# Kernel tuning notes

Hardware: AMD Instinct MI355X
Metric: run time of the kernel (lower is better)

The kernel has to match this reference:

```python
import jax, jax.numpy as jnp
import numpy as np

N = 100000
NEG_SLOPE = 0.2

def _leaky_relu(x, slope):
    return jnp.where(x >= 0, x, slope * x)

def _gat_layer(h_in, W, a_src, a_dst, b, src, dst, heads, out_ch):
    # h: [N, H, C]
    h = (h_in @ W).reshape(-1, heads, out_ch)
    alpha_src = (h * a_src).sum(-1)  # [N, H]
    alpha_dst = (h * a_dst).sum(-1)  # [N, H]
    e = _leaky_relu(alpha_src[src] + alpha_dst[dst], NEG_SLOPE)  # [E, H]
    # segment softmax over destination nodes
    m = jax.ops.segment_max(e, dst, num_segments=N)
    m = jnp.where(jnp.isfinite(m), m, 0.0)
    ex = jnp.exp(e - m[dst])
    denom = jax.ops.segment_sum(ex, dst, num_segments=N)
    attn = ex / (denom[dst] + 1e-16)  # [E, H]
    out = jax.ops.segment_sum(h[src] * attn[:, :, None], dst, num_segments=N)  # [N, H, C]
    return out.reshape(-1, heads * out_ch) + b

def setup_inputs() -> dict:
    key = jax.random.key(0)
    ks = jax.random.split(key, 10)
    F_in, H1, C1, n_cls = 512, 8, 8, 16
    E = 1600000
    x = jax.random.normal(ks[0], (N, F_in), dtype=jnp.float32)
    edge_index = jax.random.randint(ks[1], (2, E), 0, N, dtype=jnp.int64)
    s1 = 1.0 / np.sqrt(F_in)
    W1 = jax.random.uniform(ks[2], (F_in, H1 * C1), jnp.float32, -s1, s1)
    a1_src = jax.random.normal(ks[3], (H1, C1), dtype=jnp.float32) * 0.1
    a1_dst = jax.random.normal(ks[4], (H1, C1), dtype=jnp.float32) * 0.1
    b1 = jnp.zeros((H1 * C1,), jnp.float32)
    s2 = 1.0 / np.sqrt(H1 * C1)
    W2 = jax.random.uniform(ks[5], (H1 * C1, n_cls), jnp.float32, -s2, s2)
    a2_src = jax.random.normal(ks[6], (1, n_cls), dtype=jnp.float32) * 0.1
    a2_dst = jax.random.normal(ks[7], (1, n_cls), dtype=jnp.float32) * 0.1
    b2 = jnp.zeros((n_cls,), jnp.float32)
    return {"x": x, "edge_index": edge_index, "W1": W1, "a1_src": a1_src,
            "a1_dst": a1_dst, "b1": b1, "W2": W2, "a2_src": a2_src,
            "a2_dst": a2_dst, "b2": b2}

def reference(x, edge_index, W1, a1_src, a1_dst, b1, W2, a2_src, a2_dst, b2):
    # add self loops (GATConv default)
    loops = jnp.arange(N, dtype=edge_index.dtype)
    src = jnp.concatenate([edge_index[0], loops])
    dst = jnp.concatenate([edge_index[1], loops])
    h = _gat_layer(x, W1, a1_src, a1_dst, b1, src, dst, 8, 8)
    h = jax.nn.elu(h)
    out = _gat_layer(h, W2, a2_src, a2_dst, b2, src, dst, 1, 16)
    return jax.nn.log_softmax(out, axis=1)
```

## Files before the change

kernel.cpp:

```cpp
#include <hip/hip_runtime.h>
#include <math.h>

#define NEG_SLOPE 0.2f
#define BKT_SHIFT 8
#define BKT_RANGE 256
#define EPB 4096

typedef __attribute__((ext_vector_type(8))) short bf16x8;
typedef __attribute__((ext_vector_type(4))) float f32x4;

__device__ __forceinline__ float elu1(float x)  { return x > 0.f ? x : expm1f(x); }

__device__ __forceinline__ unsigned short f2bf(float f) {
  unsigned u = __float_as_uint(f);
  unsigned r = (u + 0x7FFFu + ((u >> 16) & 1u)) >> 16;
  return (unsigned short)r;
}
__device__ __forceinline__ float bf2f(unsigned short s) {
  return __uint_as_float((unsigned)s << 16);
}
__device__ __forceinline__ float bflo(unsigned u) { return __uint_as_float(u << 16); }
__device__ __forceinline__ float bfhi(unsigned u) { return __uint_as_float(u & 0xFFFF0000u); }
__device__ __forceinline__ unsigned cvt_pk_bf16(float lo, float hi) {
  unsigned r;
  asm("v_cvt_pk_bf16_f32 %0, %1, %2" : "=v"(r) : "v"(lo), "v"(hi));
  return r;
}

__global__ __launch_bounds__(256) void k_cvtW(const float* __restrict__ W,
                                              unsigned short* __restrict__ Wt) {
  int i = blockIdx.x * 256 + threadIdx.x;
  if (i >= 512 * 64) return;
  int k = i >> 6, c = i & 63;
  Wt[(size_t)c * 512 + k] = f2bf(W[i]);
}

__global__ __launch_bounds__(256) void k_gemm1_mfma(const float* __restrict__ x,
                                                    const unsigned short* __restrict__ Wt,
                                                    unsigned short* __restrict__ h1b, int N) {
  __shared__ unsigned short As[128 * 64];
  __shared__ unsigned short Bs[64 * 64];
  const int t = threadIdx.x;
  const int w = t >> 6;
  const int l = t & 63;
  const int fr = l & 15;
  const int fq = l >> 4;
  const int rowbase = blockIdx.x * 128;
  f32x4 acc[2][4] = {};

  for (int k0 = 0; k0 < 512; k0 += 64) {
#pragma unroll
    for (int j = 0; j < 8; ++j) {
      int idx = j * 256 + t;
      int row = idx >> 4;
      int cg  = idx & 15;
      int grow = rowbase + row;
      float4 v = make_float4(0.f, 0.f, 0.f, 0.f);
      if (grow < N) v = *(const float4*)(x + (size_t)grow * 512 + k0 + cg * 4);
      uint2 pk;
      pk.x = cvt_pk_bf16(v.x, v.y);
      pk.y = cvt_pk_bf16(v.z, v.w);
      int ch = cg >> 1;
      int pch = ch ^ (row & 7);
      *((uint2*)(As + row * 64 + pch * 8 + (cg & 1) * 4)) = pk;
    }
#pragma unroll
    for (int rep = 0; rep < 2; ++rep) {
      int i = t + rep * 256;
      int c = i >> 3, ch = i & 7;
      uint4 v = *(const uint4*)(Wt + (size_t)c * 512 + k0 + ch * 8);
      *((uint4*)(Bs + c * 64 + (ch ^ (c & 7)) * 8)) = v;
    }
    __syncthreads();
#pragma unroll
    for (int ks = 0; ks < 2; ++ks) {
      bf16x8 a[2], b[4];
#pragma unroll
      for (int m = 0; m < 2; ++m) {
        int r = w * 32 + m * 16 + fr;
        int ch = (ks * 4 + fq) ^ (r & 7);
        a[m] = *((const bf16x8*)(As + r * 64 + ch * 8));
      }
#pragma unroll
      for (int n = 0; n < 4; ++n) {
        int c = n * 16 + fr;
        int ch = (ks * 4 + fq) ^ (c & 7);
        b[n] = *((const bf16x8*)(Bs + c * 64 + ch * 8));
      }
#pragma unroll
      for (int m = 0; m < 2; ++m)
#pragma unroll
        for (int n = 0; n < 4; ++n)
          acc[m][n] = __builtin_amdgcn_mfma_f32_16x16x32_bf16(a[m], b[n], acc[m][n], 0, 0, 0);
    }
    __syncthreads();
  }
#pragma unroll
  for (int m = 0; m < 2; ++m) {
    int rb = rowbase + w * 32 + m * 16 + fq * 4;
#pragma unroll
    for (int reg = 0; reg < 4; ++reg) {
      int row = rb + reg;
      if (row < N) {
#pragma unroll
        for (int n = 0; n < 4; ++n)
          h1b[(size_t)row * 64 + n * 16 + fr] = f2bf(acc[m][n][reg]);
      }
    }
  }
}

__global__ __launch_bounds__(256) void k_alpha1(const unsigned short* __restrict__ h1b,
                                                const float* __restrict__ a1s,
                                                const float* __restrict__ a1d,
                                                float* __restrict__ ef1s,
                                                float* __restrict__ ef1d, int N) {
  int idx = blockIdx.x * blockDim.x + threadIdx.x;
  if (idx >= N * 8) return;
  int h = idx & 7;
  uint4 raw = *(const uint4*)(h1b + (size_t)idx * 8);
  float v[8];
  v[0] = bflo(raw.x); v[1] = bfhi(raw.x);
  v[2] = bflo(raw.y); v[3] = bfhi(raw.y);
  v[4] = bflo(raw.z); v[5] = bfhi(raw.z);
  v[6] = bflo(raw.w); v[7] = bfhi(raw.w);
  const float* s_ = a1s + h * 8;
  const float* d_ = a1d + h * 8;
  float ss = 0.f, dd = 0.f;
#pragma unroll
  for (int j = 0; j < 8; ++j) { ss += v[j] * s_[j]; dd += v[j] * d_[j]; }
  *(float2*)(ef1s + (size_t)idx * 2) = make_float2(expf(ss), expf(NEG_SLOPE * ss));
  *(float2*)(ef1d + (size_t)idx * 2) = make_float2(expf(dd), expf(NEG_SLOPE * dd));
}

__global__ __launch_bounds__(512) void k_zero(int* __restrict__ p, int n) {
  int i = blockIdx.x * blockDim.x + threadIdx.x;
  if (i < n) p[i] = 0;
}

__global__ __launch_bounds__(256) void k_bhist(const int* __restrict__ dst,
                                               int* __restrict__ bucketCount,
                                               int E, int B) {
  __shared__ int h[512];
  int t = threadIdx.x;
  for (int i = t; i < B; i += 256) h[i] = 0;
  __syncthreads();
  int e0 = blockIdx.x * EPB;
#pragma unroll
  for (int i = 0; i < EPB / 256; ++i) {
    int e = e0 + i * 256 + t;
    if (e < E) atomicAdd(&h[dst[e] >> BKT_SHIFT], 1);
  }
  __syncthreads();
  for (int i = t; i < B; i += 256)
    if (h[i]) atomicAdd(bucketCount + i, h[i]);
}

__global__ __launch_bounds__(512) void k_bscan(const int* __restrict__ bucketCount,
                                               int* __restrict__ bucketOff,
                                               int* __restrict__ gCursor, int B, int E) {
  __shared__ int sm[512];
  int t = threadIdx.x;
  int v = (t < B) ? bucketCount[t] : 0;
  sm[t] = v;
  __syncthreads();
  int acc = v;
#pragma unroll
  for (int o = 1; o < 512; o <<= 1) {
    int u = (t >= o) ? sm[t - o] : 0;
    __syncthreads();
    acc += u;
    sm[t] = acc;
    __syncthreads();
  }
  if (t < B) {
    bucketOff[t] = acc - v;
    gCursor[t] = acc - v;
  }
  if (t == 0) bucketOff[B] = E;
}

__global__ __launch_bounds__(256) void k_bin(const int* __restrict__ src,
                                             const int* __restrict__ dst,
                                             int* __restrict__ gCursor,
                                             unsigned* __restrict__ binned,
                                             int E, int B) {
  __shared__ int hist[512];
  __shared__ int base[512];
  int t = threadIdx.x;
  for (int i = t; i < B; i += 256) hist[i] = 0;
  __syncthreads();
  int e0 = blockIdx.x * EPB;
#pragma unroll
  for (int i = 0; i < EPB / 256; ++i) {
    int e = e0 + i * 256 + t;
    if (e < E) atomicAdd(&hist[dst[e] >> BKT_SHIFT], 1);
  }
  __syncthreads();
  for (int i = t; i < B; i += 256) {
    int c = hist[i];
    base[i] = c ? atomicAdd(gCursor + i, c) : 0;
    hist[i] = 0;
  }
  __syncthreads();
#pragma unroll
  for (int i = 0; i < EPB / 256; ++i) {
    int e = e0 + i * 256 + t;
    if (e < E) {
      int d = dst[e];
      int b = d >> BKT_SHIFT;
      int r = atomicAdd(&hist[b], 1);
      binned[base[b] + r] = ((unsigned)(d & (BKT_RANGE - 1)) << 24) | (unsigned)src[e];
    }
  }
}

__global__ __launch_bounds__(256) void k_build(const int* __restrict__ bucketOff,
                                               const unsigned* __restrict__ binned,
                                               int* __restrict__ rowptr,
                                               int* __restrict__ deg,
                                               int* __restrict__ srt, int N) {
  __shared__ int ldeg[BKT_RANGE];
  __shared__ int sm[BKT_RANGE];
  __shared__ int lcur[BKT_RANGE];
  int t = threadIdx.x;
  int b = blockIdx.x;
  int nbase = b * BKT_RANGE;
  int estart = bucketOff[b];
  int eend = bucketOff[b + 1];
  ldeg[t] = 0;
  __syncthreads();
  for (int e = estart + t; e < eend; e += 256)
    atomicAdd(&ldeg[binned[e] >> 24], 1);
  __syncthreads();
  int v = ldeg[t];
  sm[t] = v;
  __syncthreads();
  int acc = v;
#pragma unroll
  for (int o = 1; o < 256; o <<= 1) {
    int u = (t >= o) ? sm[t - o] : 0;
    __syncthreads();
    acc += u;
    sm[t] = acc;
    __syncthreads();
  }
  int excl = estart + acc - v;
  int node = nbase + t;
  if (node < N) {
    rowptr[node] = excl;
    deg[node] = v;
  }
  lcur[t] = excl;
  __syncthreads();
  for (int e = estart + t; e < eend; e += 256) {
    unsigned p = binned[e];
    int pos = atomicAdd(&lcur[p >> 24], 1);
    srt[pos] = (int)(p & 0xFFFFFFu);
  }
}

__global__ __launch_bounds__(256) void k_agg1f(const int* __restrict__ rowptr,
                                               const int* __restrict__ deg,
                                               const int* __restrict__ srt,
                                               const float* __restrict__ ef1s,
                                               const float* __restrict__ ef1d,
                                               const unsigned short* __restrict__ h1b,
                                               const float* __restrict__ b1,
                                               const float* __restrict__ W2,
                                               const float* __restrict__ a2s,
                                               const float* __restrict__ a2d,
                                               unsigned short* __restrict__ h2b,
                                               float* __restrict__ ef2s,
                                               float* __restrict__ ef2d, int N) {
  __shared__ float vsm[4][64];
  const int t = threadIdx.x;
  const int w = t >> 6;
  const int lane = t & 63;
  const int wid = blockIdx.x * 4 + w;
  const int slot = lane >> 4;
  const int c4 = lane & 15;
  const int h = c4 >> 1;
  float a2sr = a2s[c4];
  float a2dr = a2d[c4];
  float wreg[16];
#pragma unroll
  for (int m = 0; m < 16; ++m) wreg[m] = W2[(slot * 16 + m) * 16 + c4];
  float4 b1v = *(const float4*)(b1 + c4 * 4);
  if (wid >= N) return;
  const int d = wid;

  float2 ddv = *(const float2*)(ef1d + (size_t)d * 16 + h * 2);
  float2 psv = *(const float2*)(ef1s + (size_t)d * 16 + h * 2);
  uint2 sv = *(const uint2*)(h1b + (size_t)d * 64 + c4 * 4);
  float ex0 = fmaxf(psv.x * ddv.x, psv.y * ddv.y);
  ex0 = (slot == 0) ? ex0 : 0.f;
  float a0 = ex0 * bflo(sv.x), a1 = ex0 * bfhi(sv.x);
  float a2 = ex0 * bflo(sv.y), a3 = ex0 * bfhi(sv.y);
  float den = ex0;

  int start = rowptr[d];
  int len = deg[d];
  for (int k = 0; k < len; k += 4) {
    int idx = k + slot;
    bool valid = idx < len;
    int s = d;
    if (valid) s = srt[start + idx];
    float2 p = *(const float2*)(ef1s + (size_t)s * 16 + h * 2);
    uint2 hv = *(const uint2*)(h1b + (size_t)s * 64 + c4 * 4);
    float ex = fmaxf(p.x * ddv.x, p.y * ddv.y);
    ex = valid ? ex : 0.f;
    a0 = fmaf(ex, bflo(hv.x), a0);
    a1 = fmaf(ex, bfhi(hv.x), a1);
    a2 = fmaf(ex, bflo(hv.y), a2);
    a3 = fmaf(ex, bfhi(hv.y), a3);
    den += ex;
  }
#pragma unroll
  for (int o = 16; o < 64; o <<= 1) {
    a0 += __shfl_xor(a0, o);
    a1 += __shfl_xor(a1, o);
    a2 += __shfl_xor(a2, o);
    a3 += __shfl_xor(a3, o);
    den += __shfl_xor(den, o);
  }
  float rden = 1.f / (den + 1e-16f);
  if (slot == 0) {
    float4 vv;
    vv.x = elu1(a0 * rden + b1v.x);
    vv.y = elu1(a1 * rden + b1v.y);
    vv.z = elu1(a2 * rden + b1v.z);
    vv.w = elu1(a3 * rden + b1v.w);
    *(float4*)&vsm[w][c4 * 4] = vv;
  }
  float partial = 0.f;
#pragma unroll
  for (int m = 0; m < 16; ++m) partial = fmaf(vsm[w][slot * 16 + m], wreg[m], partial);
  float qs = partial * a2sr;
  float qd = partial * a2dr;
#pragma unroll
  for (int o = 1; o < 64; o <<= 1) {
    qs += __shfl_xor(qs, o);
    qd += __shfl_xor(qd, o);
  }
  float p2 = partial + __shfl_down(partial, 32);
  float hcv = p2 + __shfl_down(p2, 16);
  if (lane < 16) h2b[(size_t)d * 16 + c4] = f2bf(hcv);
  if (lane == 0) {
    *(float2*)(ef2s + (size_t)d * 2) = make_float2(expf(qs), expf(NEG_SLOPE * qs));
    *(float2*)(ef2d + (size_t)d * 2) = make_float2(expf(qd), expf(NEG_SLOPE * qd));
  }
}

__global__ __launch_bounds__(256) void k_agg2(const int* __restrict__ rowptr,
                                              const int* __restrict__ deg,
                                              const int* __restrict__ srt,
                                              const float* __restrict__ ef2s,
                                              const float* __restrict__ ef2d,
                                              const unsigned short* __restrict__ h2b,
                                              const float* __restrict__ b2,
                                              float* __restrict__ out, int N) {
  const int t = threadIdx.x;
  const int lane = t & 63;
  const int wid = (blockIdx.x * 256 + t) >> 6;
  const int slot = lane >> 2;
  const int cg = lane & 3;
  float4 b2v = *(const float4*)(b2 + cg * 4);
  if (wid >= N) return;
  const int d = wid;
  float2 ddp = *(const float2*)(ef2d + (size_t)d * 2);
  float2 ps0 = *(const float2*)(ef2s + (size_t)d * 2);
  uint2 sv = *(const uint2*)(h2b + (size_t)d * 16 + cg * 4);
  float ex0 = fmaxf(ps0.x * ddp.x, ps0.y * ddp.y);
  ex0 = (slot == 0) ? ex0 : 0.f;
  float a0 = ex0 * bflo(sv.x), a1 = ex0 * bfhi(sv.x);
  float a2 = ex0 * bflo(sv.y), a3 = ex0 * bfhi(sv.y);
  float den = ex0;

  int start = rowptr[d];
  int len = deg[d];
  for (int k = 0; k < len; k += 16) {
    int idx = k + slot;
    bool valid = idx < len;
    int s = d;
    if (valid) s = srt[start + idx];
    float2 p = *(const float2*)(ef2s + (size_t)s * 2);
    uint2 hv = *(const uint2*)(h2b + (size_t)s * 16 + cg * 4);
    float ex = fmaxf(p.x * ddp.x, p.y * ddp.y);
    ex = valid ? ex : 0.f;
    a0 = fmaf(ex, bflo(hv.x), a0);
    a1 = fmaf(ex, bfhi(hv.x), a1);
    a2 = fmaf(ex, bflo(hv.y), a2);
    a3 = fmaf(ex, bfhi(hv.y), a3);
    den += ex;
  }
#pragma unroll
  for (int o = 4; o < 64; o <<= 1) {
    a0 += __shfl_xor(a0, o);
    a1 += __shfl_xor(a1, o);
    a2 += __shfl_xor(a2, o);
    a3 += __shfl_xor(a3, o);
    den += __shfl_xor(den, o);
  }
  float rden = 1.f / (den + 1e-16f);
  float v0 = a0 * rden + b2v.x;
  float v1 = a1 * rden + b2v.y;
  float v2 = a2 * rden + b2v.z;
  float v3 = a3 * rden + b2v.w;
  float m = fmaxf(fmaxf(v0, v1), fmaxf(v2, v3));
  m = fmaxf(m, __shfl_xor(m, 1));
  m = fmaxf(m, __shfl_xor(m, 2));
  float s = expf(v0 - m) + expf(v1 - m) + expf(v2 - m) + expf(v3 - m);
  s += __shfl_xor(s, 1);
  s += __shfl_xor(s, 2);
  float lse = m + logf(s);
  if (lane < 4) {
    float4 o4 = make_float4(v0 - lse, v1 - lse, v2 - lse, v3 - lse);
    *(float4*)(out + (size_t)d * 16 + cg * 4) = o4;
  }
}

extern "C" void kernel_launch(void* const* d_in, const int* in_sizes, int n_in,
                              void* d_out, int out_size, void* d_ws, size_t ws_size,
                              hipStream_t stream) {
  const float* x    = (const float*)d_in[0];
  const int*   ei   = (const int*)d_in[1];
  const float* W1   = (const float*)d_in[2];
  const float* a1s  = (const float*)d_in[3];
  const float* a1d  = (const float*)d_in[4];
  const float* b1   = (const float*)d_in[5];
  const float* W2   = (const float*)d_in[6];
  const float* a2s  = (const float*)d_in[7];
  const float* a2d  = (const float*)d_in[8];
  const float* b2   = (const float*)d_in[9];
  float* out = (float*)d_out;

  const int N = in_sizes[0] / 512;
  const int E = in_sizes[1] / 2;
  const int* src = ei;
  const int* dst = ei + E;
  const int B = (N + BKT_RANGE - 1) >> BKT_SHIFT;
  const int EB = (E + EPB - 1) / EPB;

  float* w = (float*)d_ws;
  float* ef1s = w;  w += (size_t)N * 16;
  float* ef1d = w;  w += (size_t)N * 16;
  float* ef2s = w;  w += (size_t)N * 2;
  float* ef2d = w;  w += (size_t)N * 2;
  unsigned short* h1b = (unsigned short*)w;  w += (size_t)N * 32;
  unsigned short* h2b = (unsigned short*)w;  w += (size_t)N * 8;
  unsigned short* Wt  = (unsigned short*)w;  w += 512 * 64 / 2;
  int* iw = (int*)w;
  int* deg         = iw;  iw += N;
  int* rowptr      = iw;  iw += N;
  int* bucketCount = iw;  iw += 1024;
  int* bucketOff   = iw;  iw += 1024;
  int* gCursor     = iw;  iw += 1024;
  int* srt         = iw;  iw += E;
  unsigned* binned = (unsigned*)iw;  iw += E;

  k_zero<<<2, 512, 0, stream>>>(bucketCount, 1024);
  k_bhist<<<EB, 256, 0, stream>>>(dst, bucketCount, E, B);
  k_bscan<<<1, 512, 0, stream>>>(bucketCount, bucketOff, gCursor, B, E);
  k_bin<<<EB, 256, 0, stream>>>(src, dst, gCursor, binned, E, B);
  k_build<<<B, 256, 0, stream>>>(bucketOff, binned, rowptr, deg, srt, N);

  k_cvtW<<<(512 * 64 + 255) / 256, 256, 0, stream>>>(W1, Wt);
  k_gemm1_mfma<<<(N + 127) / 128, 256, 0, stream>>>(x, Wt, h1b, N);
  k_alpha1<<<(N * 8 + 255) / 256, 256, 0, stream>>>(h1b, a1s, a1d, ef1s, ef1d, N);
  k_agg1f<<<(N + 3) / 4, 256, 0, stream>>>(rowptr, deg, srt, ef1s, ef1d, h1b,
                                           b1, W2, a2s, a2d, h2b, ef2s, ef2d, N);

  k_agg2<<<(N + 3) / 4, 256, 0, stream>>>(rowptr, deg, srt, ef2s, ef2d, h2b, b2, out, N);
}
```

Measured before the change: 253.3 us.

## Store layer-1 features as FP8 and source attention exps as packed BF16

k_alpha1 now also writes the layer-1 node features in FP8 (e4m3), and both layers store the source-side exp terms as packed BF16 pairs instead of float2. The gather-heavy aggregation kernels then read half as many bytes per neighbor for these arrays. The zeroing of bucket counts is folded into the weight-conversion kernel, which removes one launch. The cost is lower precision: FP8 features and BF16 exponentials may push the output past the accuracy tolerance.

```diff
diff --git a/kernel.cpp b/kernel.cpp
--- a/kernel.cpp
+++ b/kernel.cpp
@@ -15,9 +15,6 @@
   unsigned u = __float_as_uint(f);
   unsigned r = (u + 0x7FFFu + ((u >> 16) & 1u)) >> 16;
   return (unsigned short)r;
-}
-__device__ __forceinline__ float bf2f(unsigned short s) {
-  return __uint_as_float((unsigned)s << 16);
 }
 __device__ __forceinline__ float bflo(unsigned u) { return __uint_as_float(u << 16); }
 __device__ __forceinline__ float bfhi(unsigned u) { return __uint_as_float(u & 0xFFFF0000u); }
@@ -27,9 +24,11 @@
   return r;
 }
 
-__global__ __launch_bounds__(256) void k_cvtW(const float* __restrict__ W,
-                                              unsigned short* __restrict__ Wt) {
+__global__ __launch_bounds__(256) void k_cvtW_zero(const float* __restrict__ W,
+                                                   unsigned short* __restrict__ Wt,
+                                                   int* __restrict__ bucketCount) {
   int i = blockIdx.x * 256 + threadIdx.x;
+  if (i < 1024) bucketCount[i] = 0;
   if (i >= 512 * 64) return;
   int k = i >> 6, c = i & 63;
   Wt[(size_t)c * 512 + k] = f2bf(W[i]);
@@ -113,8 +112,9 @@
 __global__ __launch_bounds__(256) void k_alpha1(const unsigned short* __restrict__ h1b,
                                                 const float* __restrict__ a1s,
                                                 const float* __restrict__ a1d,
-                                                float* __restrict__ ef1s,
-                                                float* __restrict__ ef1d, int N) {
+                                                unsigned* __restrict__ ef1sp,
+                                                float* __restrict__ ef1d,
+                                                unsigned* __restrict__ h1f8, int N) {
   int idx = blockIdx.x * blockDim.x + threadIdx.x;
   if (idx >= N * 8) return;
   int h = idx & 7;
@@ -129,13 +129,14 @@
   float ss = 0.f, dd = 0.f;
 #pragma unroll
   for (int j = 0; j < 8; ++j) { ss += v[j] * s_[j]; dd += v[j] * d_[j]; }
-  *(float2*)(ef1s + (size_t)idx * 2) = make_float2(expf(ss), expf(NEG_SLOPE * ss));
+  ef1sp[idx] = cvt_pk_bf16(expf(ss), expf(NEG_SLOPE * ss));
   *(float2*)(ef1d + (size_t)idx * 2) = make_float2(expf(dd), expf(NEG_SLOPE * dd));
-}
-
-__global__ __launch_bounds__(512) void k_zero(int* __restrict__ p, int n) {
-  int i = blockIdx.x * blockDim.x + threadIdx.x;
-  if (i < n) p[i] = 0;
+  unsigned lo = 0, hi = 0;
+  lo = __builtin_amdgcn_cvt_pk_fp8_f32(v[0], v[1], lo, 0);
+  lo = __builtin_amdgcn_cvt_pk_fp8_f32(v[2], v[3], lo, 1);
+  hi = __builtin_amdgcn_cvt_pk_fp8_f32(v[4], v[5], hi, 0);
+  hi = __builtin_amdgcn_cvt_pk_fp8_f32(v[6], v[7], hi, 1);
+  *(uint2*)(h1f8 + (size_t)idx * 2) = make_uint2(lo, hi);
 }
 
 __global__ __launch_bounds__(256) void k_bhist(const int* __restrict__ dst,
@@ -263,15 +264,15 @@
 __global__ __launch_bounds__(256) void k_agg1f(const int* __restrict__ rowptr,
                                                const int* __restrict__ deg,
                                                const int* __restrict__ srt,
-                                               const float* __restrict__ ef1s,
+                                               const unsigned* __restrict__ ef1sp,
                                                const float* __restrict__ ef1d,
-                                               const unsigned short* __restrict__ h1b,
+                                               const unsigned* __restrict__ h1f8,
                                                const float* __restrict__ b1,
                                                const float* __restrict__ W2,
                                                const float* __restrict__ a2s,
                                                const float* __restrict__ a2d,
                                                unsigned short* __restrict__ h2b,
-                                               float* __restrict__ ef2s,
+                                               unsigned* __restrict__ ef2sp,
                                                float* __restrict__ ef2d, int N) {
   __shared__ float vsm[4][64];
   const int t = threadIdx.x;
@@ -291,12 +292,14 @@
   const int d = wid;
 
   float2 ddv = *(const float2*)(ef1d + (size_t)d * 16 + h * 2);
-  float2 psv = *(const float2*)(ef1s + (size_t)d * 16 + h * 2);
-  uint2 sv = *(const uint2*)(h1b + (size_t)d * 64 + c4 * 4);
-  float ex0 = fmaxf(psv.x * ddv.x, psv.y * ddv.y);
+  unsigned es0 = ef1sp[(size_t)d * 8 + h];
+  unsigned sv = h1f8[(size_t)d * 16 + c4];
+  float ex0 = fmaxf(bflo(es0) * ddv.x, bfhi(es0) * ddv.y);
   ex0 = (slot == 0) ? ex0 : 0.f;
-  float a0 = ex0 * bflo(sv.x), a1 = ex0 * bfhi(sv.x);
-  float a2 = ex0 * bflo(sv.y), a3 = ex0 * bfhi(sv.y);
+  float a0 = ex0 * __builtin_amdgcn_cvt_f32_fp8(sv, 0);
+  float a1 = ex0 * __builtin_amdgcn_cvt_f32_fp8(sv, 1);
+  float a2 = ex0 * __builtin_amdgcn_cvt_f32_fp8(sv, 2);
+  float a3 = ex0 * __builtin_amdgcn_cvt_f32_fp8(sv, 3);
   float den = ex0;
 
   int start = rowptr[d];
@@ -306,14 +309,14 @@
     bool valid = idx < len;
     int s = d;
     if (valid) s = srt[start + idx];
-    float2 p = *(const float2*)(ef1s + (size_t)s * 16 + h * 2);
-    uint2 hv = *(const uint2*)(h1b + (size_t)s * 64 + c4 * 4);
-    float ex = fmaxf(p.x * ddv.x, p.y * ddv.y);
+    unsigned es = ef1sp[(size_t)s * 8 + h];
+    unsigned hv = h1f8[(size_t)s * 16 + c4];
+    float ex = fmaxf(bflo(es) * ddv.x, bfhi(es) * ddv.y);
     ex = valid ? ex : 0.f;
-    a0 = fmaf(ex, bflo(hv.x), a0);
-    a1 = fmaf(ex, bfhi(hv.x), a1);
-    a2 = fmaf(ex, bflo(hv.y), a2);
-    a3 = fmaf(ex, bfhi(hv.y), a3);
+    a0 = fmaf(ex, __builtin_amdgcn_cvt_f32_fp8(hv, 0), a0);
+    a1 = fmaf(ex, __builtin_amdgcn_cvt_f32_fp8(hv, 1), a1);
+    a2 = fmaf(ex, __builtin_amdgcn_cvt_f32_fp8(hv, 2), a2);
+    a3 = fmaf(ex, __builtin_amdgcn_cvt_f32_fp8(hv, 3), a3);
     den += ex;
   }
 #pragma unroll
@@ -347,7 +350,7 @@
   float hcv = p2 + __shfl_down(p2, 16);
   if (lane < 16) h2b[(size_t)d * 16 + c4] = f2bf(hcv);
   if (lane == 0) {
-    *(float2*)(ef2s + (size_t)d * 2) = make_float2(expf(qs), expf(NEG_SLOPE * qs));
+    ef2sp[d] = cvt_pk_bf16(expf(qs), expf(NEG_SLOPE * qs));
     *(float2*)(ef2d + (size_t)d * 2) = make_float2(expf(qd), expf(NEG_SLOPE * qd));
   }
 }
@@ -355,7 +358,7 @@
 __global__ __launch_bounds__(256) void k_agg2(const int* __restrict__ rowptr,
                                               const int* __restrict__ deg,
                                               const int* __restrict__ srt,
-                                              const float* __restrict__ ef2s,
+                                              const unsigned* __restrict__ ef2sp,
                                               const float* __restrict__ ef2d,
                                               const unsigned short* __restrict__ h2b,
                                               const float* __restrict__ b2,
@@ -369,9 +372,9 @@
   if (wid >= N) return;
   const int d = wid;
   float2 ddp = *(const float2*)(ef2d + (size_t)d * 2);
-  float2 ps0 = *(const float2*)(ef2s + (size_t)d * 2);
+  unsigned ps0 = ef2sp[d];
   uint2 sv = *(const uint2*)(h2b + (size_t)d * 16 + cg * 4);
-  float ex0 = fmaxf(ps0.x * ddp.x, ps0.y * ddp.y);
+  float ex0 = fmaxf(bflo(ps0) * ddp.x, bfhi(ps0) * ddp.y);
   ex0 = (slot == 0) ? ex0 : 0.f;
   float a0 = ex0 * bflo(sv.x), a1 = ex0 * bfhi(sv.x);
   float a2 = ex0 * bflo(sv.y), a3 = ex0 * bfhi(sv.y);
@@ -384,9 +387,9 @@
     bool valid = idx < len;
     int s = d;
     if (valid) s = srt[start + idx];
-    float2 p = *(const float2*)(ef2s + (size_t)s * 2);
+    unsigned ps = ef2sp[s];
     uint2 hv = *(const uint2*)(h2b + (size_t)s * 16 + cg * 4);
-    float ex = fmaxf(p.x * ddp.x, p.y * ddp.y);
+    float ex = fmaxf(bflo(ps) * ddp.x, bfhi(ps) * ddp.y);
     ex = valid ? ex : 0.f;
     a0 = fmaf(ex, bflo(hv.x), a0);
     a1 = fmaf(ex, bfhi(hv.x), a1);
@@ -443,10 +446,11 @@
   const int EB = (E + EPB - 1) / EPB;
 
   float* w = (float*)d_ws;
-  float* ef1s = w;  w += (size_t)N * 16;
   float* ef1d = w;  w += (size_t)N * 16;
-  float* ef2s = w;  w += (size_t)N * 2;
   float* ef2d = w;  w += (size_t)N * 2;
+  unsigned* ef1sp = (unsigned*)w;  w += (size_t)N * 8;
+  unsigned* ef2sp = (unsigned*)w;  w += (size_t)N;
+  unsigned* h1f8  = (unsigned*)w;  w += (size_t)N * 16;
   unsigned short* h1b = (unsigned short*)w;  w += (size_t)N * 32;
   unsigned short* h2b = (unsigned short*)w;  w += (size_t)N * 8;
   unsigned short* Wt  = (unsigned short*)w;  w += 512 * 64 / 2;
@@ -459,17 +463,17 @@
   int* srt         = iw;  iw += E;
   unsigned* binned = (unsigned*)iw;  iw += E;
 
-  k_zero<<<2, 512, 0, stream>>>(bucketCount, 1024);
+  k_cvtW_zero<<<(512 * 64 + 255) / 256, 256, 0, stream>>>(W1, Wt, bucketCount);
+
   k_bhist<<<EB, 256, 0, stream>>>(dst, bucketCount, E, B);
   k_bscan<<<1, 512, 0, stream>>>(bucketCount, bucketOff, gCursor, B, E);
   k_bin<<<EB, 256, 0, stream>>>(src, dst, gCursor, binned, E, B);
   k_build<<<B, 256, 0, stream>>>(bucketOff, binned, rowptr, deg, srt, N);
 
-  k_cvtW<<<(512 * 64 + 255) / 256, 256, 0, stream>>>(W1, Wt);
   k_gemm1_mfma<<<(N + 127) / 128, 256, 0, stream>>>(x, Wt, h1b, N);
-  k_alpha1<<<(N * 8 + 255) / 256, 256, 0, stream>>>(h1b, a1s, a1d, ef1s, ef1d, N);
-  k_agg1f<<<(N + 3) / 4, 256, 0, stream>>>(rowptr, deg, srt, ef1s, ef1d, h1b,
-                                           b1, W2, a2s, a2d, h2b, ef2s, ef2d, N);
-
-  k_agg2<<<(N + 3) / 4, 256, 0, stream>>>(rowptr, deg, srt, ef2s, ef2d, h2b, b2, out, N);
-}
+  k_alpha1<<<(N * 8 + 255) / 256, 256, 0, stream>>>(h1b, a1s, a1d, ef1sp, ef1d, h1f8, N);
+  k_agg1f<<<(N + 3) / 4, 256, 0, stream>>>(rowptr, deg, srt, ef1sp, ef1d, h1f8,
+                                           b1, W2, a2s, a2d, h2b, ef2sp, ef2d, N);
+
+  k_agg2<<<(N + 3) / 4, 256, 0, stream>>>(rowptr, deg, srt, ef2sp, ef2d, h2b, b2, out, N);
+}
```

Measured after the change: 242.3 us. -4.3%, faster.
